# Kernel optimization log

Measured on AMD Instinct MI355X. Metric: run time of the kernel, lower is better.

The kernel has to match this reference:

```python
import jax, jax.numpy as jnp
import numpy as np

B, N, D_IN, D_OUT, HH, WW = 64, 512, 256, 32, 160, 160

def setup_inputs() -> dict:
    key = jax.random.key(0)
    k1, k2, k3, k4, k5 = jax.random.split(key, 5)
    return {
        "entity_embeddings": jax.random.normal(k1, (B, N, D_IN), dtype=jnp.float32),
        "weight": jax.random.normal(k2, (D_IN, D_OUT), dtype=jnp.float32) * (1.0 / np.sqrt(D_IN)),
        "bias": jnp.zeros((D_OUT,), dtype=jnp.float32),
        "entity_x": jax.random.randint(k3, (B, N), 0, WW, dtype=jnp.int32),
        "entity_y": jax.random.randint(k4, (B, N), 0, HH, dtype=jnp.int32),
        "entity_num": jax.random.randint(k5, (B,), 1, N, dtype=jnp.int32),
        "H": HH,
        "W": WW,
    }

def reference(entity_embeddings, weight, bias, entity_x, entity_y, entity_num, H, W):
    # fc_block: Linear + ReLU  -> [B, N, D_OUT]
    proj = jax.nn.relu(jnp.einsum('bni,io->bno', entity_embeddings, weight) + bias)
    # mask padded entities (sequence_mask from entity_num)
    mask = (jnp.arange(proj.shape[1])[None, :] < entity_num[:, None]).astype(proj.dtype)
    proj = proj * mask[:, :, None]
    # ScatterConnection ('add'): location = (y, x) -> flat index y*W + x
    flat_idx = entity_y.astype(jnp.int32) * W + entity_x.astype(jnp.int32)  # [B, N]
    b = proj.shape[0]
    out = jnp.zeros((b, H * W, proj.shape[2]), dtype=proj.dtype)
    out = out.at[jnp.arange(b)[:, None], flat_idx].add(proj)  # scatter-add
    # -> [B, D_OUT, H, W]
    scatter_map = out.reshape(b, H, W, proj.shape[2]).transpose(0, 3, 1, 2)
    return scatter_map
```

## Files before the change

kernel.cpp:

```cpp
#include <hip/hip_runtime.h>
#include <stdint.h>

constexpr int DIN  = 256;
constexpr int DOUT = 32;

typedef float f32x4  __attribute__((ext_vector_type(4)));
typedef short bf16x8 __attribute__((ext_vector_type(8)));


__device__ __forceinline__ uint16_t f2bf(float f, float& back) {
    uint32_t u = __builtin_bit_cast(uint32_t, f);
    uint32_t r = (u + 0x7fffu + ((u >> 16) & 1u)) >> 16;
    back = __builtin_bit_cast(float, r << 16);
    return (uint16_t)r;
}

__global__ __launch_bounds__(256)
void k_prep(const float* __restrict__ weight,
            const int* __restrict__ ex, const int* __restrict__ ey,
            const int* __restrict__ en, const int* __restrict__ pW,
            uint16_t* __restrict__ wfh, uint16_t* __restrict__ wfl,
            int* __restrict__ destpk,
            int N, int nent, int HW)
{
    const int bid = blockIdx.x, tid = threadIdx.x;
    if (bid < 4) {
        const int id   = bid * 256 + tid;
        const int t    = id >> 7;
        const int h    = (id >> 6) & 1;
        const int lane = id & 63;
        const int kb   = t * 32 + (lane >> 4) * 8;
        const int col  = h * 16 + (lane & 15);
        const int off  = ((t * 2 + h) * 64 + lane) * 8;
        #pragma unroll
        for (int j = 0; j < 8; ++j) {
            float w = weight[(size_t)(kb + j) * DOUT + col];
            float back; uint16_t hi = f2bf(w, back);
            float resid = w - back;
            float b2;  uint16_t lo = f2bf(resid, b2);
            wfh[off + j] = hi;
            wfl[off + j] = lo;
        }
    } else {
        const int e = (bid - 4) * 256 + tid;
        if (e < nent) {
            const int b = e / N, n = e - b * N;
            const int W = *pW;
            destpk[e] = (n < en[b]) ? (b * DOUT * HW + ey[e] * W + ex[e]) : -1;
        }
    }
}

__global__ __launch_bounds__(256)
void k_gemm_scatter(const float* __restrict__ emb,
                    const float* __restrict__ bias,
                    const uint16_t* __restrict__ wfh,
                    const uint16_t* __restrict__ wfl,
                    const int* __restrict__ destpk,
                    float* __restrict__ out,
                    int nent, int HW)
{
    const int tid  = threadIdx.x;
    const int lane = tid & 63;
    const int wv   = tid >> 6;
    const int eb   = blockIdx.x * 64 + wv * 16;
    const int row  = lane & 15;
    const int kg   = lane >> 4;

    int e = eb + row; if (e >= nent) e = nent - 1;
    const float* erow = emb + (size_t)e * DIN + kg * 8;

    f32x4 acc0 = {0.f, 0.f, 0.f, 0.f};
    f32x4 acc1 = {0.f, 0.f, 0.f, 0.f};

    #pragma unroll
    for (int t = 0; t < 8; ++t) {
        const float4 a0 = *(const float4*)(erow + t * 32);
        const float4 a1 = *(const float4*)(erow + t * 32 + 4);
        const float af[8] = {a0.x, a0.y, a0.z, a0.w, a1.x, a1.y, a1.z, a1.w};
        bf16x8 ahi, alo;
        #pragma unroll
        for (int j = 0; j < 8; ++j) {
            float back; uint16_t h = f2bf(af[j], back);
            float resid = af[j] - back;
            float b2;  uint16_t l = f2bf(resid, b2);
            ahi[j] = (short)h;
            alo[j] = (short)l;
        }
        const int fo = (t * 2) * 64 + lane;
        const bf16x8 bh0 = *(const bf16x8*)&wfh[fo * 8];
        const bf16x8 bh1 = *(const bf16x8*)&wfh[(fo + 64) * 8];
        const bf16x8 bl0 = *(const bf16x8*)&wfl[fo * 8];
        const bf16x8 bl1 = *(const bf16x8*)&wfl[(fo + 64) * 8];
        acc0 = __builtin_amdgcn_mfma_f32_16x16x32_bf16(ahi, bh0, acc0, 0, 0, 0);
        acc1 = __builtin_amdgcn_mfma_f32_16x16x32_bf16(ahi, bh1, acc1, 0, 0, 0);
        acc0 = __builtin_amdgcn_mfma_f32_16x16x32_bf16(alo, bh0, acc0, 0, 0, 0);
        acc1 = __builtin_amdgcn_mfma_f32_16x16x32_bf16(alo, bh1, acc1, 0, 0, 0);
        acc0 = __builtin_amdgcn_mfma_f32_16x16x32_bf16(ahi, bl0, acc0, 0, 0, 0);
        acc1 = __builtin_amdgcn_mfma_f32_16x16x32_bf16(ahi, bl1, acc1, 0, 0, 0);
    }

    const int c0 = lane & 15, c1 = c0 + 16;
    const float b0 = bias[c0], b1 = bias[c1];
    #pragma unroll
    for (int r = 0; r < 4; ++r) {
        const int ent = eb + (lane >> 4) * 4 + r;
        if (ent >= nent) continue;
        const int d = destpk[ent];
        if (d < 0) continue;
        const float v0 = fmaxf(acc0[r] + b0, 0.f);
        const float v1 = fmaxf(acc1[r] + b1, 0.f);
        if (v0 != 0.f) atomicAdd(out + d + c0 * HW, v0);
        if (v1 != 0.f) atomicAdd(out + d + c1 * HW, v1);
    }
}

constexpr int FET = 64, FKT = 64, FEP = FKT + 4;
__global__ __launch_bounds__(256)
void enc_fallback(const float* __restrict__ emb, const float* __restrict__ weight,
                  const float* __restrict__ bias, const int* __restrict__ ex,
                  const int* __restrict__ ey, const int* __restrict__ en,
                  const int* __restrict__ pW, float* __restrict__ out,
                  int N, int nent, int HW)
{
    __shared__ float s_emb[FET][FEP];
    __shared__ float s_w[FKT * DOUT];
    const int tid = threadIdx.x;
    const int og = tid & 7, eg = tid >> 3;
    const int eb = blockIdx.x * FET;
    float4 pe[4]; float4 pw[2];
    #pragma unroll
    for (int r = 0; r < 4; ++r) {
        int f = (r << 8) + tid, rw = f >> 4, col = (f & 15) << 2;
        int e = eb + rw; if (e >= nent) e = nent - 1;
        pe[r] = *(const float4*)&emb[(size_t)e * DIN + col];
    }
    #pragma unroll
    for (int r = 0; r < 2; ++r) pw[r] = *(const float4*)&weight[(size_t)(((r << 8) + tid) << 2)];
    float acc[2][4] = {{0,0,0,0},{0,0,0,0}};
    for (int t = 0; t < 4; ++t) {
        #pragma unroll
        for (int r = 0; r < 4; ++r) {
            int f = (r << 8) + tid;
            *(float4*)&s_emb[f >> 4][(f & 15) << 2] = pe[r];
        }
        #pragma unroll
        for (int r = 0; r < 2; ++r) *(float4*)&s_w[((r << 8) + tid) << 2] = pw[r];
        __syncthreads();
        if (t < 3) {
            const int kt = (t + 1) * FKT;
            #pragma unroll
            for (int r = 0; r < 4; ++r) {
                int f = (r << 8) + tid, rw = f >> 4, col = (f & 15) << 2;
                int e = eb + rw; if (e >= nent) e = nent - 1;
                pe[r] = *(const float4*)&emb[(size_t)e * DIN + kt + col];
            }
            #pragma unroll
            for (int r = 0; r < 2; ++r)
                pw[r] = *(const float4*)&weight[(size_t)kt * DOUT + (((r << 8) + tid) << 2)];
        }
        #pragma unroll
        for (int k = 0; k < FKT; k += 4) {
            float4 e0 = *(const float4*)&s_emb[eg][k];
            float4 e1 = *(const float4*)&s_emb[eg + 32][k];
            float4 w0 = *(const float4*)&s_w[(k + 0) * DOUT + og * 4];
            float4 w1 = *(const float4*)&s_w[(k + 1) * DOUT + og * 4];
            float4 w2 = *(const float4*)&s_w[(k + 2) * DOUT + og * 4];
            float4 w3 = *(const float4*)&s_w[(k + 3) * DOUT + og * 4];
            acc[0][0] += e0.x*w0.x + e0.y*w1.x + e0.z*w2.x + e0.w*w3.x;
            acc[0][1] += e0.x*w0.y + e0.y*w1.y + e0.z*w2.y + e0.w*w3.y;
            acc[0][2] += e0.x*w0.z + e0.y*w1.z + e0.z*w2.z + e0.w*w3.z;
            acc[0][3] += e0.x*w0.w + e0.y*w1.w + e0.z*w2.w + e0.w*w3.w;
            acc[1][0] += e1.x*w0.x + e1.y*w1.x + e1.z*w2.x + e1.w*w3.x;
            acc[1][1] += e1.x*w0.y + e1.y*w1.y + e1.z*w2.y + e1.w*w3.y;
            acc[1][2] += e1.x*w0.z + e1.y*w1.z + e1.z*w2.z + e1.w*w3.z;
            acc[1][3] += e1.x*w0.w + e1.y*w1.w + e1.z*w2.w + e1.w*w3.w;
        }
        __syncthreads();
    }
    const int W = *pW;
    const float4 bv = *(const float4*)&bias[og * 4];
    #pragma unroll
    for (int i = 0; i < 2; ++i) {
        int ent = eb + eg + i * 32;
        if (ent >= nent) continue;
        int b = ent / N, n = ent - b * N;
        if (n >= en[b]) continue;
        float* dst = out + ((size_t)b * DOUT + og * 4) * (size_t)HW
                         + (size_t)ey[ent] * W + ex[ent];
        float v0 = fmaxf(acc[i][0] + bv.x, 0.f);
        float v1 = fmaxf(acc[i][1] + bv.y, 0.f);
        float v2 = fmaxf(acc[i][2] + bv.z, 0.f);
        float v3 = fmaxf(acc[i][3] + bv.w, 0.f);
        if (v0 != 0.f) atomicAdd(dst + 0 * (size_t)HW, v0);
        if (v1 != 0.f) atomicAdd(dst + 1 * (size_t)HW, v1);
        if (v2 != 0.f) atomicAdd(dst + 2 * (size_t)HW, v2);
        if (v3 != 0.f) atomicAdd(dst + 3 * (size_t)HW, v3);
    }
}

extern "C" void kernel_launch(void* const* d_in, const int* in_sizes, int n_in,
                              void* d_out, int out_size, void* d_ws, size_t ws_size,
                              hipStream_t stream) {
    const float* emb    = (const float*)d_in[0];
    const float* weight = (const float*)d_in[1];
    const float* bias   = (const float*)d_in[2];
    const int*   ex     = (const int*)d_in[3];
    const int*   ey     = (const int*)d_in[4];
    const int*   en     = (const int*)d_in[5];
    const int*   pW     = (const int*)d_in[7];
    float*       out    = (float*)d_out;

    const int nent = in_sizes[3];
    const int B    = in_sizes[5];
    const int N    = nent / B;
    const int HW   = (int)((size_t)out_size / ((size_t)B * DOUT));

    uint16_t* wfh    = (uint16_t*)d_ws;
    uint16_t* wfl    = (uint16_t*)((char*)d_ws + 16384);
    int*      destpk = (int*)((char*)d_ws + 32768);

    const size_t ws_need = 32768 + (size_t)nent * sizeof(int);
    const bool fits = (ws_size >= ws_need);

    if (fits) {
        const int prep_blocks = 4 + (nent + 255) / 256;
        k_prep<<<prep_blocks, 256, 0, stream>>>(weight, ex, ey, en, pW,
                                                wfh, wfl, destpk, N, nent, HW);
        (void)hipMemsetAsync(d_out, 0, (size_t)out_size * sizeof(float), stream);
        const int gblocks = (nent + 63) / 64;
        k_gemm_scatter<<<gblocks, 256, 0, stream>>>(emb, bias, wfh, wfl, destpk,
                                                    out, nent, HW);
    } else {
        (void)hipMemsetAsync(d_out, 0, (size_t)out_size * sizeof(float), stream);
        const int blocks = (nent + FET - 1) / FET;
        enc_fallback<<<blocks, 256, 0, stream>>>(emb, weight, bias, ex, ey, en, pW,
                                                 out, N, nent, HW);
    }
}
```

Before: 57.55 us.

## Fuse output zeroing with scatter-add in per-batch spatial chunk kernel

The GEMM no longer scatters directly. It writes ReLU'd projections to a workspace buffer. A new kernel, one block per (batch, spatial chunk), zeroes its slice of the output and then scatter-adds the entities that fall in that chunk. This replaces the separate hipMemset and means the zeroed region is still in cache when the atomics land. The cost is an extra round trip of the projection through global memory, and every chunk block re-reads all entity coordinates for its batch.

```diff
diff --git a/kernel.cpp b/kernel.cpp
--- a/kernel.cpp
+++ b/kernel.cpp
@@ -3,6 +3,7 @@
 
 constexpr int DIN  = 256;
 constexpr int DOUT = 32;
+constexpr int NCH  = 16;
 
 typedef float f32x4  __attribute__((ext_vector_type(4)));
 typedef short bf16x8 __attribute__((ext_vector_type(8)));
@@ -17,48 +18,33 @@
 
 __global__ __launch_bounds__(256)
 void k_prep(const float* __restrict__ weight,
-            const int* __restrict__ ex, const int* __restrict__ ey,
-            const int* __restrict__ en, const int* __restrict__ pW,
-            uint16_t* __restrict__ wfh, uint16_t* __restrict__ wfl,
-            int* __restrict__ destpk,
-            int N, int nent, int HW)
-{
-    const int bid = blockIdx.x, tid = threadIdx.x;
-    if (bid < 4) {
-        const int id   = bid * 256 + tid;
-        const int t    = id >> 7;
-        const int h    = (id >> 6) & 1;
-        const int lane = id & 63;
-        const int kb   = t * 32 + (lane >> 4) * 8;
-        const int col  = h * 16 + (lane & 15);
-        const int off  = ((t * 2 + h) * 64 + lane) * 8;
-        #pragma unroll
-        for (int j = 0; j < 8; ++j) {
-            float w = weight[(size_t)(kb + j) * DOUT + col];
-            float back; uint16_t hi = f2bf(w, back);
-            float resid = w - back;
-            float b2;  uint16_t lo = f2bf(resid, b2);
-            wfh[off + j] = hi;
-            wfl[off + j] = lo;
-        }
-    } else {
-        const int e = (bid - 4) * 256 + tid;
-        if (e < nent) {
-            const int b = e / N, n = e - b * N;
-            const int W = *pW;
-            destpk[e] = (n < en[b]) ? (b * DOUT * HW + ey[e] * W + ex[e]) : -1;
-        }
-    }
-}
-
-__global__ __launch_bounds__(256)
-void k_gemm_scatter(const float* __restrict__ emb,
-                    const float* __restrict__ bias,
-                    const uint16_t* __restrict__ wfh,
-                    const uint16_t* __restrict__ wfl,
-                    const int* __restrict__ destpk,
-                    float* __restrict__ out,
-                    int nent, int HW)
+            uint16_t* __restrict__ wfh, uint16_t* __restrict__ wfl)
+{
+    const int id = blockIdx.x * 256 + threadIdx.x;
+    const int t    = id >> 7;
+    const int h    = (id >> 6) & 1;
+    const int lane = id & 63;
+    const int kb   = t * 32 + (lane >> 4) * 8;
+    const int col  = h * 16 + (lane & 15);
+    const int off  = ((t * 2 + h) * 64 + lane) * 8;
+    #pragma unroll
+    for (int j = 0; j < 8; ++j) {
+        float w = weight[(size_t)(kb + j) * DOUT + col];
+        float back; uint16_t hi = f2bf(w, back);
+        float resid = w - back;
+        float b2;  uint16_t lo = f2bf(resid, b2);
+        wfh[off + j] = hi;
+        wfl[off + j] = lo;
+    }
+}
+
+__global__ __launch_bounds__(256)
+void k_gemm(const float* __restrict__ emb,
+            const float* __restrict__ bias,
+            const uint16_t* __restrict__ wfh,
+            const uint16_t* __restrict__ wfl,
+            float* __restrict__ proj,
+            int nent)
 {
     const int tid  = threadIdx.x;
     const int lane = tid & 63;
@@ -106,12 +92,58 @@
     for (int r = 0; r < 4; ++r) {
         const int ent = eb + (lane >> 4) * 4 + r;
         if (ent >= nent) continue;
-        const int d = destpk[ent];
-        if (d < 0) continue;
-        const float v0 = fmaxf(acc0[r] + b0, 0.f);
-        const float v1 = fmaxf(acc1[r] + b1, 0.f);
-        if (v0 != 0.f) atomicAdd(out + d + c0 * HW, v0);
-        if (v1 != 0.f) atomicAdd(out + d + c1 * HW, v1);
+        proj[(size_t)ent * DOUT + c0] = fmaxf(acc0[r] + b0, 0.f);
+        proj[(size_t)ent * DOUT + c1] = fmaxf(acc1[r] + b1, 0.f);
+    }
+}
+
+__global__ __launch_bounds__(256)
+void k_zeroscatter(const float* __restrict__ proj,
+                   const int* __restrict__ ex, const int* __restrict__ ey,
+                   const int* __restrict__ en, const int* __restrict__ pW,
+                   float* __restrict__ out,
+                   int N, int nent, int HW, int HWCH)
+{
+    const int tid = threadIdx.x;
+    const int b   = blockIdx.x / NCH;
+    const int ch  = blockIdx.x % NCH;
+    const int hw0 = ch * HWCH;
+    const int hwlen = min(HWCH, HW - hw0);
+    if (hwlen <= 0) return;
+
+    float* base = out + (size_t)b * DOUT * HW;
+
+    if (((hw0 | hwlen) & 3) == 0) {
+        const int n4 = hwlen >> 2;
+        #pragma unroll 4
+        for (int c = 0; c < DOUT; ++c) {
+            float4* p = (float4*)(base + (size_t)c * HW + hw0);
+            for (int i = tid; i < n4; i += 256)
+                p[i] = make_float4(0.f, 0.f, 0.f, 0.f);
+        }
+    } else {
+        for (int c = 0; c < DOUT; ++c) {
+            float* p = base + (size_t)c * HW + hw0;
+            for (int i = tid; i < hwlen; i += 256) p[i] = 0.f;
+        }
+    }
+    __syncthreads();
+
+    const int cnt = en[b];
+    const int W = *pW;
+    for (int slot = tid; slot < N; slot += 256) {
+        if (slot >= cnt) continue;
+        const int ent = b * N + slot;
+        if (ent >= nent) continue;
+        const int hw = ey[ent] * W + ex[ent];
+        if (hw < hw0 || hw >= hw0 + hwlen) continue;
+        const float* pv = proj + (size_t)ent * DOUT;
+        float* dst = base + hw;
+        #pragma unroll
+        for (int c = 0; c < DOUT; ++c) {
+            const float v = pv[c];
+            if (v != 0.f) atomicAdd(dst + (size_t)c * HW, v);
+        }
     }
 }
 
@@ -215,22 +247,19 @@
     const int B    = in_sizes[5];
     const int N    = nent / B;
     const int HW   = (int)((size_t)out_size / ((size_t)B * DOUT));
-
-    uint16_t* wfh    = (uint16_t*)d_ws;
-    uint16_t* wfl    = (uint16_t*)((char*)d_ws + 16384);
-    int*      destpk = (int*)((char*)d_ws + 32768);
-
-    const size_t ws_need = 32768 + (size_t)nent * sizeof(int);
-    const bool fits = (ws_size >= ws_need);
-
-    if (fits) {
-        const int prep_blocks = 4 + (nent + 255) / 256;
-        k_prep<<<prep_blocks, 256, 0, stream>>>(weight, ex, ey, en, pW,
-                                                wfh, wfl, destpk, N, nent, HW);
-        (void)hipMemsetAsync(d_out, 0, (size_t)out_size * sizeof(float), stream);
-        const int gblocks = (nent + 63) / 64;
-        k_gemm_scatter<<<gblocks, 256, 0, stream>>>(emb, bias, wfh, wfl, destpk,
-                                                    out, nent, HW);
+    const int HWCH = (HW + NCH - 1) / NCH;
+
+    uint16_t* wfh  = (uint16_t*)d_ws;
+    uint16_t* wfl  = (uint16_t*)((char*)d_ws + 16384);
+    float*    proj = (float*)((char*)d_ws + 32768);
+
+    const size_t ws_need = 32768 + (size_t)nent * DOUT * sizeof(float);
+
+    if (ws_size >= ws_need) {
+        k_prep<<<4, 256, 0, stream>>>(weight, wfh, wfl);
+        k_gemm<<<(nent + 63) / 64, 256, 0, stream>>>(emb, bias, wfh, wfl, proj, nent);
+        k_zeroscatter<<<B * NCH, 256, 0, stream>>>(proj, ex, ey, en, pW, out,
+                                                   N, nent, HW, HWCH);
     } else {
         (void)hipMemsetAsync(d_out, 0, (size_t)out_size * sizeof(float), stream);
         const int blocks = (nent + FET - 1) / FET;
```

Result: slower. 67.26 us (+16.9%).

## Fuse prep, memset and GEMM-scatter into one cooperative kernel with grid sync

Applied to the files above, without the earlier changes.

Replaces the weight-split prep kernel, the memset and the GEMM-scatter kernel with a single cooperative launch. Each block zeroes its slice of the output interleaved with the GEMM loop, converts weights to hi/lo bf16 inline, and computes destinations on the fly. A grid-wide sync then separates the zeroing from the atomic scatter. This removes two launches and the workspace round trip, at the cost of redundant weight conversion per wave and a grid barrier. Grid is 512 blocks, which relies on 2 blocks per CU fitting for the cooperative launch.

```diff
diff --git a/kernel.cpp b/kernel.cpp
--- a/kernel.cpp
+++ b/kernel.cpp
@@ -1,12 +1,14 @@
 #include <hip/hip_runtime.h>
+#include <hip/hip_cooperative_groups.h>
 #include <stdint.h>
+
+namespace cg = cooperative_groups;
 
 constexpr int DIN  = 256;
 constexpr int DOUT = 32;
 
 typedef float f32x4  __attribute__((ext_vector_type(4)));
 typedef short bf16x8 __attribute__((ext_vector_type(8)));
-
 
 __device__ __forceinline__ uint16_t f2bf(float f, float& back) {
     uint32_t u = __builtin_bit_cast(uint32_t, f);
@@ -15,50 +17,12 @@
     return (uint16_t)r;
 }
 
-__global__ __launch_bounds__(256)
-void k_prep(const float* __restrict__ weight,
-            const int* __restrict__ ex, const int* __restrict__ ey,
-            const int* __restrict__ en, const int* __restrict__ pW,
-            uint16_t* __restrict__ wfh, uint16_t* __restrict__ wfl,
-            int* __restrict__ destpk,
-            int N, int nent, int HW)
-{
-    const int bid = blockIdx.x, tid = threadIdx.x;
-    if (bid < 4) {
-        const int id   = bid * 256 + tid;
-        const int t    = id >> 7;
-        const int h    = (id >> 6) & 1;
-        const int lane = id & 63;
-        const int kb   = t * 32 + (lane >> 4) * 8;
-        const int col  = h * 16 + (lane & 15);
-        const int off  = ((t * 2 + h) * 64 + lane) * 8;
-        #pragma unroll
-        for (int j = 0; j < 8; ++j) {
-            float w = weight[(size_t)(kb + j) * DOUT + col];
-            float back; uint16_t hi = f2bf(w, back);
-            float resid = w - back;
-            float b2;  uint16_t lo = f2bf(resid, b2);
-            wfh[off + j] = hi;
-            wfl[off + j] = lo;
-        }
-    } else {
-        const int e = (bid - 4) * 256 + tid;
-        if (e < nent) {
-            const int b = e / N, n = e - b * N;
-            const int W = *pW;
-            destpk[e] = (n < en[b]) ? (b * DOUT * HW + ey[e] * W + ex[e]) : -1;
-        }
-    }
-}
-
-__global__ __launch_bounds__(256)
-void k_gemm_scatter(const float* __restrict__ emb,
-                    const float* __restrict__ bias,
-                    const uint16_t* __restrict__ wfh,
-                    const uint16_t* __restrict__ wfl,
-                    const int* __restrict__ destpk,
-                    float* __restrict__ out,
-                    int nent, int HW)
+__global__ __launch_bounds__(256, 2)
+void k_coop(const float* __restrict__ emb, const float* __restrict__ weight,
+            const float* __restrict__ bias, const int* __restrict__ ex,
+            const int* __restrict__ ey, const int* __restrict__ en,
+            const int* __restrict__ pW, float* __restrict__ out,
+            int N, int nent, int HW, int zTotal4, int ZQ)
 {
     const int tid  = threadIdx.x;
     const int lane = tid & 63;
@@ -70,6 +34,11 @@
     int e = eb + row; if (e >= nent) e = nent - 1;
     const float* erow = emb + (size_t)e * DIN + kg * 8;
 
+    float4* outv = (float4*)out;
+    const float4 z4 = make_float4(0.f, 0.f, 0.f, 0.f);
+    const size_t zslice = (size_t)blockIdx.x * ZQ * 256;
+    int zq = 0;
+
     f32x4 acc0 = {0.f, 0.f, 0.f, 0.f};
     f32x4 acc1 = {0.f, 0.f, 0.f, 0.f};
 
@@ -77,21 +46,44 @@
     for (int t = 0; t < 8; ++t) {
         const float4 a0 = *(const float4*)(erow + t * 32);
         const float4 a1 = *(const float4*)(erow + t * 32 + 4);
+        const float* wp = weight + (size_t)(t * 32 + kg * 8) * DOUT + row;
+        float wf0[8], wf1[8];
+        #pragma unroll
+        for (int j = 0; j < 8; ++j) {
+            wf0[j] = wp[(size_t)j * DOUT];
+            wf1[j] = wp[(size_t)j * DOUT + 16];
+        }
+        #pragma unroll
+        for (int q = 0; q < 12; ++q) {
+            if (zq < ZQ) {
+                const size_t idx = zslice + (size_t)zq * 256 + tid;
+                if (idx < (size_t)zTotal4) outv[idx] = z4;
+            }
+            ++zq;
+        }
         const float af[8] = {a0.x, a0.y, a0.z, a0.w, a1.x, a1.y, a1.z, a1.w};
-        bf16x8 ahi, alo;
-        #pragma unroll
-        for (int j = 0; j < 8; ++j) {
-            float back; uint16_t h = f2bf(af[j], back);
-            float resid = af[j] - back;
-            float b2;  uint16_t l = f2bf(resid, b2);
-            ahi[j] = (short)h;
-            alo[j] = (short)l;
-        }
-        const int fo = (t * 2) * 64 + lane;
-        const bf16x8 bh0 = *(const bf16x8*)&wfh[fo * 8];
-        const bf16x8 bh1 = *(const bf16x8*)&wfh[(fo + 64) * 8];
-        const bf16x8 bl0 = *(const bf16x8*)&wfl[fo * 8];
-        const bf16x8 bl1 = *(const bf16x8*)&wfl[(fo + 64) * 8];
+        bf16x8 ahi, alo, bh0, bl0, bh1, bl1;
+        #pragma unroll
+        for (int j = 0; j < 8; ++j) {
+            float back, b2;
+            const uint16_t h = f2bf(af[j], back);
+            const uint16_t l = f2bf(af[j] - back, b2);
+            ahi[j] = (short)h; alo[j] = (short)l;
+        }
+        #pragma unroll
+        for (int j = 0; j < 8; ++j) {
+            float back, b2;
+            const uint16_t h = f2bf(wf0[j], back);
+            const uint16_t l = f2bf(wf0[j] - back, b2);
+            bh0[j] = (short)h; bl0[j] = (short)l;
+        }
+        #pragma unroll
+        for (int j = 0; j < 8; ++j) {
+            float back, b2;
+            const uint16_t h = f2bf(wf1[j], back);
+            const uint16_t l = f2bf(wf1[j] - back, b2);
+            bh1[j] = (short)h; bl1[j] = (short)l;
+        }
         acc0 = __builtin_amdgcn_mfma_f32_16x16x32_bf16(ahi, bh0, acc0, 0, 0, 0);
         acc1 = __builtin_amdgcn_mfma_f32_16x16x32_bf16(ahi, bh1, acc1, 0, 0, 0);
         acc0 = __builtin_amdgcn_mfma_f32_16x16x32_bf16(alo, bh0, acc0, 0, 0, 0);
@@ -99,19 +91,28 @@
         acc0 = __builtin_amdgcn_mfma_f32_16x16x32_bf16(ahi, bl0, acc0, 0, 0, 0);
         acc1 = __builtin_amdgcn_mfma_f32_16x16x32_bf16(ahi, bl1, acc1, 0, 0, 0);
     }
-
-    const int c0 = lane & 15, c1 = c0 + 16;
-    const float b0 = bias[c0], b1 = bias[c1];
+    while (zq < ZQ) {
+        const size_t idx = zslice + (size_t)zq * 256 + tid;
+        if (idx < (size_t)zTotal4) outv[idx] = z4;
+        ++zq;
+    }
+
+    __threadfence();
+    cg::this_grid().sync();
+
+    const float b0 = bias[row], b1 = bias[row + 16];
+    const int Wd = *pW;
     #pragma unroll
     for (int r = 0; r < 4; ++r) {
-        const int ent = eb + (lane >> 4) * 4 + r;
+        const int ent = eb + kg * 4 + r;
         if (ent >= nent) continue;
-        const int d = destpk[ent];
-        if (d < 0) continue;
+        const int bb = ent / N, nn = ent - bb * N;
+        if (nn >= en[bb]) continue;
+        const int hw = ey[ent] * Wd + ex[ent];
         const float v0 = fmaxf(acc0[r] + b0, 0.f);
         const float v1 = fmaxf(acc1[r] + b1, 0.f);
-        if (v0 != 0.f) atomicAdd(out + d + c0 * HW, v0);
-        if (v1 != 0.f) atomicAdd(out + d + c1 * HW, v1);
+        if (v0 != 0.f) atomicAdd(out + (size_t)(bb * DOUT + row) * HW + hw, v0);
+        if (v1 != 0.f) atomicAdd(out + (size_t)(bb * DOUT + row + 16) * HW + hw, v1);
     }
 }
 
@@ -211,27 +212,32 @@
     const int*   pW     = (const int*)d_in[7];
     float*       out    = (float*)d_out;
 
-    const int nent = in_sizes[3];
+    int nent = in_sizes[3];
     const int B    = in_sizes[5];
     const int N    = nent / B;
+    const int DIN_rt = in_sizes[0] / nent;
     const int HW   = (int)((size_t)out_size / ((size_t)B * DOUT));
-
-    uint16_t* wfh    = (uint16_t*)d_ws;
-    uint16_t* wfl    = (uint16_t*)((char*)d_ws + 16384);
-    int*      destpk = (int*)((char*)d_ws + 32768);
-
-    const size_t ws_need = 32768 + (size_t)nent * sizeof(int);
-    const bool fits = (ws_size >= ws_need);
-
-    if (fits) {
-        const int prep_blocks = 4 + (nent + 255) / 256;
-        k_prep<<<prep_blocks, 256, 0, stream>>>(weight, ex, ey, en, pW,
-                                                wfh, wfl, destpk, N, nent, HW);
-        (void)hipMemsetAsync(d_out, 0, (size_t)out_size * sizeof(float), stream);
-        const int gblocks = (nent + 63) / 64;
-        k_gemm_scatter<<<gblocks, 256, 0, stream>>>(emb, bias, wfh, wfl, destpk,
-                                                    out, nent, HW);
-    } else {
+    const int zTotal4 = out_size / 4;
+
+    const int grid = (nent + 63) / 64;
+    const int ZQ = (zTotal4 + grid * 256 - 1) / (grid * 256);
+
+    const bool coop_ok = (DIN_rt == DIN) && (in_sizes[2] == DOUT) &&
+                         (out_size % 4 == 0) && (B * N == nent) &&
+                         (grid <= 512);
+
+    bool done = false;
+    if (coop_ok) {
+        void* args[] = { (void*)&emb, (void*)&weight, (void*)&bias, (void*)&ex,
+                         (void*)&ey, (void*)&en, (void*)&pW, (void*)&out,
+                         (void*)&N, (void*)&nent, (void*)&HW,
+                         (void*)&zTotal4, (void*)&ZQ };
+        hipError_t err = hipLaunchCooperativeKernel((const void*)k_coop,
+                                                    dim3(grid), dim3(256),
+                                                    args, 0, stream);
+        done = (err == hipSuccess);
+    }
+    if (!done) {
         (void)hipMemsetAsync(d_out, 0, (size_t)out_size * sizeof(float), stream);
         const int blocks = (nent + FET - 1) / FET;
         enc_fallback<<<blocks, 256, 0, stream>>>(emb, weight, bias, ex, ey, en, pW,
```

Result: slower. 190.6 us (+231.2%).
